# Performance work log

Hardware: AMD Instinct MI355X
Metric: run time of the kernel (lower is better)

## Reference

```python
import math
import jax, jax.numpy as jnp
import numpy as np

GRAIN = 300   # bilinear / grain dim (gpconv output channels)
PAD = 4       # explicit zero padding before each conv1d / conv2d
POOL = 40     # adaptive pool target (mf_model_pool_dim)

def conv1d_k2(x, w, b):
    # x: [B, L, Cin], w: [Cout, Cin, 2] -> [B, L-1, Cout]
    return (jnp.einsum('blc,oc->blo', x[:, :-1], w[:, :, 0])
            + jnp.einsum('blc,oc->blo', x[:, 1:], w[:, :, 1]) + b)

def kmax_last(x, k):
    # torch-style k-max pooling: top-k values along last axis, original order kept
    idx = jnp.sort(jax.lax.top_k(x, k)[1], axis=-1)
    return jnp.take_along_axis(x, idx, axis=-1)

def kmax_len(x, k):
    # k-max pooling over the length axis (axis=1) of [B, L, C]
    return jnp.swapaxes(kmax_last(jnp.swapaxes(x, 1, 2), k), 1, 2)

def adaptive_max_1d(x, out, axis):
    # torch AdaptiveMaxPool semantics along one axis; windows precomputed statically
    L = x.shape[axis]
    r = np.arange(out)
    starts = (r * L) // out
    ends = -((-(r + 1) * L) // out)
    maxw = int((ends - starts).max())
    off = starts[:, None] + np.arange(maxw)[None, :]
    mask = jnp.asarray(off < ends[:, None])
    idxs = np.minimum(off, L - 1)
    xm = jnp.moveaxis(x, axis, -1)
    g = jnp.where(mask, xm[..., idxs], -jnp.inf)
    return jnp.moveaxis(g.max(-1), -1, axis)

def conv2d_p4(x, w, b):
    y = jax.lax.conv_general_dilated(x, w, (1, 1), [(PAD, PAD), (PAD, PAD)],
                                     dimension_numbers=('NCHW', 'OIHW', 'NCHW'))
    return y + b[None, :, None, None]

def gp_tower(x, w1, b1, w2, b2, w3, b3, k1, k2):
    # multigranular conv tower: zero-pad(4) -> conv1d(k=2) -> tanh -> k-max pool
    g0 = kmax_last(x, GRAIN)                      # [B, L, 300]
    def block(z, w, b, k):
        z = jnp.pad(z, ((0, 0), (PAD, PAD), (0, 0)))
        return kmax_len(jnp.tanh(conv1d_k2(z, w, b)), k)
    p1 = block(x, w1, b1, k1)                     # [B, k1, 300]
    p2 = block(p1, w2, b2, k2)                    # [B, k2, 300]
    p3 = block(p2, w3, b3, 1)                     # [B, 1, 300]
    return jnp.concatenate([g0, p1, p2, p3], axis=1)

def _forward(query, pos_doc, neg_docs, qw1, qb1, qw2, qb2, qw3, qb3,
             dw1, db1, dw2, db2, dw3, db3, bw, bb,
             mw1, mb1, mw2, mb2, mw3, mb3, lw, lb):
    B, Lq, _ = query.shape
    S, _, Ld, _ = neg_docs.shape
    kq1, kq2 = max(4, math.ceil(2 * Lq / 3)), max(4, math.ceil(Lq / 3))
    kd1, kd2 = max(4, math.ceil(2 * Ld / 3)), max(4, math.ceil(Ld / 3))
    qg = gp_tower(query, qw1, qb1, qw2, qb2, qw3, qb3, kq1, kq2)   # [B, Nq, 300]
    docs = jnp.concatenate([pos_doc[None], neg_docs], 0).reshape((S + 1) * B, Ld, -1)
    dg = gp_tower(docs, dw1, db1, dw2, db2, dw3, db3, kd1, kd2)    # [(S+1)B, Nd, 300]
    Nq, Nd = qg.shape[1], dg.shape[1]
    dg = dg.reshape(S + 1, B, Nd, GRAIN)
    # batched bilinear matching + sigmoid (replaces the O(Nq*Nd) per-pair loop)
    qt = jnp.einsum('bqd,de->bqe', qg, bw)
    M = jax.nn.sigmoid(jnp.einsum('bqe,sbje->sbqj', qt, dg) + bb[0])
    M = M.reshape((S + 1) * B, Nq, Nd)
    x = adaptive_max_1d(adaptive_max_1d(M, POOL, 1), POOL, 2)[:, None]  # [N,1,40,40]
    for w, b in ((mw1, mb1), (mw2, mb2), (mw3, mb3)):
        x = jax.nn.sigmoid(conv2d_p4(x, w, b))
        x = adaptive_max_1d(adaptive_max_1d(x, POOL, 2), POOL, 3)
        x = x.max(axis=1, keepdims=True)          # k-max(k=1) over channels
    feat = x[:, 0]                                # [N, 40, 40]
    h = jax.nn.sigmoid(jnp.einsum('nij,j->ni', feat, lw[0]) + lb[0])
    s = jax.nn.sigmoid(h @ lw[0] + lb[0])
    return s.reshape(S + 1, B)                    # row 0 = pos-doc scores

def setup_inputs():
    ks = jax.random.split(jax.random.key(0), 26)
    def n(i, shape, s=0.05):
        return jax.random.normal(ks[i], shape, dtype=jnp.float32) * s
    return dict(
        query=jax.random.normal(ks[0], (16, 239, 1024), dtype=jnp.float32),
        pos_doc=jax.random.normal(ks[1], (16, 479, 1024), dtype=jnp.float32),
        neg_docs=jax.random.normal(ks[2], (4, 16, 479, 1024), dtype=jnp.float32),
        qw1=n(3, (300, 1024, 2)), qb1=n(4, (300,)),
        qw2=n(5, (300, 300, 2)), qb2=n(6, (300,)),
        qw3=n(7, (300, 300, 2)), qb3=n(8, (300,)),
        dw1=n(9, (300, 1024, 2)), db1=n(10, (300,)),
        dw2=n(11, (300, 300, 2)), db2=n(12, (300,)),
        dw3=n(13, (300, 300, 2)), db3=n(14, (300,)),
        bw=n(15, (300, 300)), bb=n(16, (1,)),
        mw1=n(17, (50, 1, 2, 2)), mb1=n(18, (50,)),
        mw2=n(19, (50, 1, 2, 2)), mb2=n(20, (50,)),
        mw3=n(21, (50, 1, 2, 2)), mb3=n(22, (50,)),
        lw=n(23, (1, 40)), lb=n(24, (1,)),
    )

def reference(query, pos_doc, neg_docs, qw1, qb1, qw2, qb2, qw3, qb3,
              dw1, db1, dw2, db2, dw3, db3, bw, bb,
              mw1, mb1, mw2, mb2, mw3, mb3, lw, lb):
    return _forward(query, pos_doc, neg_docs, qw1, qb1, qw2, qb2, qw3, qb3,
                    dw1, db1, dw2, db2, dw3, db3, bw, bb,
                    mw1, mb1, mw2, mb2, mw3, mb3, lw, lb)
```

## Files before the change

kernel.cpp:

```cpp
#include <hip/hip_runtime.h>
#include <hip/hip_bf16.h>
#include <math.h>

typedef unsigned long long ull;
typedef unsigned int uint;
typedef unsigned short ushort_t;

typedef short bf16x8 __attribute__((ext_vector_type(8)));
typedef float floatx4 __attribute__((ext_vector_type(4)));

__device__ inline ushort_t f2b(float f) {
    uint u = __float_as_uint(f);
    u = u + 0x7fffu + ((u >> 16) & 1u);
    return (ushort_t)(u >> 16);
}

__device__ inline uint kmap16(ushort_t u) {
    return (u & 0x8000u) ? (uint)((~u) & 0xFFFFu) : (uint)(u | 0x8000u);
}
__device__ inline ushort_t kinv16(uint k) {
    return (k & 0x8000u) ? (ushort_t)(k ^ 0x8000u) : (ushort_t)((~k) & 0xFFFFu);
}

__device__ inline void async_copy16(const void* g, void* l) {
    __builtin_amdgcn_global_load_lds(
        (const __attribute__((address_space(1))) void*)g,
        (__attribute__((address_space(3))) void*)l, 16, 0, 0);
}

__global__ void prep_w2_kernel(const float* __restrict__ w, ushort_t* __restrict__ Wb,
                               int C, int CP) {
    int CHn = CP / 32;
    int total = CHn * 2 * 20 * 512;
    for (int i = blockIdx.x * blockDim.x + threadIdx.x; i < total;
         i += gridDim.x * blockDim.x) {
        int e = i & 7;
        int lane = (i >> 3) & 63;
        int rest = i >> 9;
        int g = rest % 20;
        int tc = rest / 20;
        int t = tc & 1, c = tc >> 1;
        int o = g * 16 + (lane & 15);
        int ch = c * 32 + (lane >> 4) * 8 + e;
        float v = (o < 300 && ch < C) ? w[((size_t)o * C + ch) * 2 + t] : 0.f;
        Wb[i] = f2b(v);
    }
}

__global__ void prep_bw_kernel(const float* __restrict__ bw, ushort_t* __restrict__ bwb) {
    int i = blockIdx.x * 256 + threadIdx.x;
    if (i >= 320 * 320) return;
    int e = i / 320, d = i - e * 320;
    bwb[i] = (e < 300 && d < 300) ? f2b(bw[d * 300 + e]) : (ushort_t)0;
}

__global__ __launch_bounds__(256) void x_pad_bf16_kernel(
    const float* __restrict__ src, const float* __restrict__ src2, int split_n,
    long long s_nstr, int Lin, ushort_t* __restrict__ dst, int rows)
{
    int r = blockIdx.x, n = blockIdx.y;
    const float* sp = (split_n > 0 && n >= split_n)
                          ? src2 + (size_t)(n - split_n) * s_nstr
                          : src + (size_t)n * s_nstr;
    int g = r - 4;
    ushort_t* dp = dst + ((size_t)n * rows + r) * 1024;
    int c = threadIdx.x * 4;
    ushort4 o = {0, 0, 0, 0};
    if (g >= 0 && g < Lin) {
        float4 v = *(const float4*)&sp[(size_t)g * 1024 + c];
        o.x = f2b(v.x); o.y = f2b(v.y); o.z = f2b(v.z); o.w = f2b(v.w);
    }
    *(ushort4*)&dp[c] = o;
}

template <int CP>
__global__ __launch_bounds__(256, 2) void conv_lds_kernel(
    const ushort_t* __restrict__ xq, long long xq_nstr,
    const ushort_t* __restrict__ xd, long long xd_nstr,
    const ushort_t* __restrict__ Wq, const ushort_t* __restrict__ Wd,
    const float* __restrict__ bq, const float* __restrict__ bd,
    int Lout_q, int Lout_d, int mtiles_q,
    ushort_t* __restrict__ yt)
{
    constexpr int CH = CP / 32;
    constexpr int BUFB = 65 * 64;
    __shared__ ushort_t Abuf[3][65 * 32];

    int mt = blockIdx.x, n = blockIdx.y;
    bool isq = (n < 16);
    if (isq && mt >= mtiles_q) return;
    const ushort_t* x = isq ? xq + (size_t)n * xq_nstr
                            : xd + (size_t)(n - 16) * xd_nstr;
    const ushort_t* W = isq ? Wq : Wd;
    const float* bias = isq ? bq : bd;
    int Lout = isq ? Lout_q : Lout_d;
    int l0 = mt * 64;

    int tid = threadIdx.x, wid = tid >> 6, lane = tid & 63;
    int wn = wid * 80;
    int lrow = lane & 15, quad = lane >> 4;

    int srow = tid >> 2;
    int sslot = (tid & 3) ^ ((tid >> 3) & 3);
    const ushort_t* gMain = x + (size_t)(l0 + srow) * CP + sslot * 8;
    const ushort_t* gXtra = x + (size_t)(l0 + 64) * CP + wid * 8;

    const ushort_t* Bw = W + ((size_t)wid * 5) * 512 + lane * 8;

    int offA[2][4];
#pragma unroll
    for (int t = 0; t < 2; t++)
#pragma unroll
        for (int ms = 0; ms < 4; ms++) {
            int r = ms * 16 + lrow + t;
            offA[t][ms] = r * 64 + ((quad ^ ((r >> 1) & 3)) << 4);
        }

    floatx4 acc[4][5];
#pragma unroll
    for (int i = 0; i < 4; i++)
#pragma unroll
        for (int j = 0; j < 5; j++) acc[i][j] = (floatx4){0.f, 0.f, 0.f, 0.f};

    char* lds0 = (char*)&Abuf[0][0];

    auto STAGE = [&](int cc, int slot) {
        char* lb = lds0 + slot * BUFB;
        async_copy16(gMain + cc * 32, lb + wid * 1024);
        if (lane == 0) async_copy16(gXtra + cc * 32, lb + 4096 + wid * 16);
    };
    auto LOADB = [&](bf16x8 (&bf)[2][5], int cc) {
#pragma unroll
        for (int t = 0; t < 2; t++)
#pragma unroll
            for (int ns = 0; ns < 5; ns++)
                bf[t][ns] = *(const bf16x8*)(Bw + (size_t)((cc * 2 + t) * 20 + ns) * 512);
    };
    auto COMPUTE = [&](bf16x8 (&bf)[2][5], int rslot) {
        const char* ab = lds0 + rslot * BUFB;
        __builtin_amdgcn_s_setprio(1);
#pragma unroll
        for (int t = 0; t < 2; t++) {
            bf16x8 af[4];
#pragma unroll
            for (int ms = 0; ms < 4; ms++)
                af[ms] = *(const bf16x8*)(ab + offA[t][ms]);
#pragma unroll
            for (int ms = 0; ms < 4; ms++)
#pragma unroll
                for (int ns = 0; ns < 5; ns++)
                    acc[ms][ns] = __builtin_amdgcn_mfma_f32_16x16x32_bf16(
                        af[ms], bf[t][ns], acc[ms][ns], 0, 0, 0);
        }
        __builtin_amdgcn_s_setprio(0);
    };
    auto WAITBAR = [&]() {
        asm volatile("s_waitcnt vmcnt(10)" ::: "memory");
        __builtin_amdgcn_s_barrier();
        __builtin_amdgcn_sched_barrier(0);
    };

    bf16x8 bA[2][5], bB[2][5];

    STAGE(0, 0);
    LOADB(bA, 0);
    STAGE(1, 1);

    int sl = 0;
    for (int c = 0; c < CH; c += 2) {
        int rA = sl;
        int rB = rA + 1; if (rB == 3) rB = 0;
        int wA = rB + 1; if (wA == 3) wA = 0;
        int wB = rA;

        WAITBAR();
        LOADB(bB, c + 1);
        __builtin_amdgcn_sched_barrier(0x38F);
        if (c + 2 < CH) STAGE(c + 2, wA);
        COMPUTE(bA, rA);

        WAITBAR();
        if (c + 2 < CH) LOADB(bA, c + 2);
        __builtin_amdgcn_sched_barrier(0x38F);
        if (c + 3 < CH) STAGE(c + 3, wB);
        COMPUTE(bB, rB);

        sl = wA;
    }

    ushort_t* yp = yt + (size_t)n * (320 * 488);
#pragma unroll
    for (int ns = 0; ns < 5; ns++) {
        int o = wn + ns * 16 + lrow;
        if (o >= 300) continue;
        float bo = bias[o];
        ushort_t* orow = yp + (size_t)o * 488;
#pragma unroll
        for (int ms = 0; ms < 4; ms++) {
            int l = l0 + ms * 16 + quad * 4;
            if (l + 3 < Lout) {
                ushort4 v;
                v.x = f2b(tanhf(acc[ms][ns][0] + bo));
                v.y = f2b(tanhf(acc[ms][ns][1] + bo));
                v.z = f2b(tanhf(acc[ms][ns][2] + bo));
                v.w = f2b(tanhf(acc[ms][ns][3] + bo));
                *(ushort4*)&orow[l] = v;
            } else {
#pragma unroll
                for (int r = 0; r < 4; r++)
                    if (l + r < Lout) orow[l + r] = f2b(tanhf(acc[ms][ns][r] + bo));
            }
        }
    }
}

__global__ __launch_bounds__(256) void topk_g0_kernel(
    const ushort_t* __restrict__ src, int CC, long long s_n,
    ushort_t* __restrict__ out, long long o_n, long long o_c)
{
    __shared__ uint hist[4][257];

    int tid = threadIdx.x, wid = tid >> 6, lane = tid & 63;
    int row = blockIdx.x * 4 + wid;
    int n = row / CC, c = row - n * CC;
    const ushort_t* sp = src + (size_t)n * s_n + (size_t)c * 1024;

    const uint* sp32 = (const uint*)(sp + (size_t)lane * 16);
    uint pk[8];
    {
        uint4 va = *(const uint4*)sp32;
        uint4 vb = *(const uint4*)(sp32 + 4);
        pk[0] = va.x; pk[1] = va.y; pk[2] = va.z; pk[3] = va.w;
        pk[4] = vb.x; pk[5] = vb.y; pk[6] = vb.z; pk[7] = vb.w;
    }
    uint key[16];
#pragma unroll
    for (int i = 0; i < 8; i++) {
        uint w = pk[i];
        uint s = w & 0x80008000u;
        w ^= 0x80008000u | ((s >> 15) * 0x7fffu);
        key[2 * i] = w & 0xffffu;
        key[2 * i + 1] = w >> 16;
    }

    uint* hg = hist[wid];
    uint rem = 300, bsel = 0, T = 0;

#pragma unroll
    for (int round = 0; round < 2; round++) {
#pragma unroll
        for (int t = 0; t < 4; t++) hg[lane + t * 64] = 0;
        __builtin_amdgcn_sched_barrier(0);
        if (round == 0) {
#pragma unroll
            for (int e = 0; e < 16; e++) atomicAdd(&hg[key[e] >> 8], 1u);
        } else {
#pragma unroll
            for (int e = 0; e < 16; e++)
                if ((key[e] >> 8) == bsel) atomicAdd(&hg[key[e] & 255u], 1u);
        }
        __builtin_amdgcn_sched_barrier(0);
        uint hv[4], Sr = 0;
#pragma unroll
        for (int t = 0; t < 4; t++) { hv[t] = hg[lane * 4 + t]; Sr += hv[t]; }
        uint suf = Sr;
#pragma unroll
        for (int off = 1; off < 64; off <<= 1) {
            uint u = __shfl_down(suf, off);
            if (lane + off < 64) suf += u;
        }
        uint acc = suf - Sr;
        uint found = 0;
#pragma unroll
        for (int t = 3; t >= 0; t--) {
            uint h = hv[t];
            if (!found && acc < rem && acc + h >= rem)
                found = ((uint)(lane * 4 + t) << 16) | (rem - acc);
            acc += h;
        }
#pragma unroll
        for (int off = 1; off < 64; off <<= 1) found |= __shfl_xor(found, off);
        if (round == 0) {
            bsel = found >> 16;
            rem = found & 0xffffu;
        } else {
            T = (bsel << 8) | (found >> 16);
            rem = found & 0xffffu;
        }
        __builtin_amdgcn_sched_barrier(0);
    }

    uint gtc = 0, eqc = 0;
#pragma unroll
    for (int e = 0; e < 16; e++) {
        gtc += (key[e] > T) ? 1u : 0u;
        eqc += (key[e] == T) ? 1u : 0u;
    }
    uint pack = (gtc << 16) | eqc, incl = pack;
#pragma unroll
    for (int off = 1; off < 64; off <<= 1) {
        uint u = __shfl_up(incl, off);
        if (lane >= off) incl += u;
    }
    uint excl = incl - pack;
    uint gt_b = excl >> 16, eq_b = excl & 0xffffu;

    ushort_t* dp = out + (size_t)n * o_n + (size_t)c * o_c;
#pragma unroll
    for (int e = 0; e < 16; e++) {
        uint kk = key[e];
        if (kk > T) {
            uint pos = gt_b + (eq_b < rem ? eq_b : rem);
            dp[pos] = kinv16(kk);
            gt_b++;
        } else if (kk == T) {
            if (eq_b < rem) dp[gt_b + eq_b] = kinv16(kk);
            eq_b++;
        }
    }
}

__global__ __launch_bounds__(256) void topk_cols_kernel(
    const ushort_t* __restrict__ yt2,
    int Lq, int Ld, int kq, int kd,
    ushort_t* __restrict__ qg, int qoff,
    ushort_t* __restrict__ dg, int doff,
    ushort_t* __restrict__ pq, long long pq_nstr,
    ushort_t* __restrict__ pd, long long pd_nstr)
{
    __shared__ __align__(16) ushort_t xin[32][488];
    __shared__ __align__(16) uint hist[32 * 257];
    ushort_t* otile = (ushort_t*)hist;

    int cg = blockIdx.x, n = blockIdx.y;
    int c0 = cg * 32;
    bool isq = (n < 16);
    int L = isq ? Lq : Ld;
    int k = isq ? kq : kd;
    int nd = isq ? n : n - 16;
    int tid = threadIdx.x;

    const ushort_t* src = yt2 + (size_t)n * (320 * 488) + (size_t)c0 * 488;
    for (int i = tid; i < 32 * 61; i += 256) {
        int j = i / 61, s = i - j * 61;
        *(uint4*)&xin[j][s * 8] = *(const uint4*)&src[(size_t)j * 488 + s * 8];
    }
    __syncthreads();

    int g = tid >> 3, r = tid & 7;
    uint* hg = &hist[g * 257];
    bool cval = (c0 + g) < 300;
    int S = (L + 7) >> 3;
    int llo = r * S, lhi = llo + S;
    if (lhi > L) lhi = L;
    if (llo > L) llo = L;

    uint rem = (uint)k;
    uint bsel = 0;
    uint Tt = 0;

#pragma unroll
    for (int round = 0; round < 2; round++) {
        for (int t = r; t < 256; t += 8) hg[t] = 0;
        for (int l = llo; l < lhi; l++) {
            uint key = cval ? kmap16(xin[g][l]) : 0x8000u;
            if (round == 0)
                atomicAdd(&hg[key >> 8], 1u);
            else if ((key >> 8) == bsel)
                atomicAdd(&hg[key & 255u], 1u);
        }
        uint hv[32];
        uint Sr = 0;
        int b0 = r * 32;
#pragma unroll
        for (int t = 0; t < 32; t++) { hv[t] = hg[b0 + t]; Sr += hv[t]; }
        uint suf = Sr;
#pragma unroll
        for (int off = 1; off < 8; off <<= 1) {
            uint u = __shfl_down(suf, off);
            if (r + off < 8) suf += u;
        }
        uint acc = suf - Sr;
        uint found = 0;
#pragma unroll
        for (int t = 31; t >= 0; t--) {
            uint h = hv[t];
            if (!found && acc < rem && acc + h >= rem)
                found = ((uint)(b0 + t) << 16) | (rem - acc);
            acc += h;
        }
#pragma unroll
        for (int off = 1; off < 8; off <<= 1) found |= __shfl_xor(found, off);
        if (round == 0) {
            bsel = found >> 16;
            rem = found & 0xffffu;
        } else {
            Tt = (bsel << 8) | (found >> 16);
            rem = found & 0xffffu;
        }
    }

    uint gtc = 0, eqc = 0;
    for (int l = llo; l < lhi; l++) {
        uint key = cval ? kmap16(xin[g][l]) : 0x8000u;
        gtc += (key > Tt) ? 1u : 0u;
        eqc += (key == Tt) ? 1u : 0u;
    }
    uint pack = (gtc << 16) | eqc, incl = pack;
#pragma unroll
    for (int off = 1; off < 8; off <<= 1) {
        uint u = __shfl_up(incl, off);
        if (r >= off) incl += u;
    }
    uint excl = incl - pack;
    uint gt_b = excl >> 16, eq_b = excl & 0xffffu;

    __syncthreads();

    for (int l = llo; l < lhi; l++) {
        uint key = cval ? kmap16(xin[g][l]) : 0x8000u;
        if (key > Tt) {
            uint pos = gt_b + (eq_b < rem ? eq_b : rem);
            otile[pos * 32 + g] = kinv16(key);
            gt_b++;
        } else if (key == Tt) {
            if (eq_b < rem) otile[(gt_b + eq_b) * 32 + g] = kinv16(key);
            eq_b++;
        }
    }
    __syncthreads();

    ushort_t* d1 = isq ? qg + ((size_t)nd * 480 + qoff) * 320 + c0
                       : dg + ((size_t)nd * 960 + doff) * 320 + c0;
    ushort_t* d2 = 0;
    if (isq) { if (pq) d2 = pq + (size_t)nd * pq_nstr + 4 * 320 + c0; }
    else     { if (pd) d2 = pd + (size_t)nd * pd_nstr + 4 * 320 + c0; }

    for (int i = tid; i < k * 8; i += 256) {
        int p = i >> 3, s = i & 7;
        ushort4 v = *(ushort4*)&otile[p * 32 + s * 4];
        *(ushort4*)&d1[(size_t)p * 320 + s * 4] = v;
        if (d2) *(ushort4*)&d2[(size_t)p * 320 + s * 4] = v;
    }
}

__global__ __launch_bounds__(256) void qt_mfma_kernel(
    const ushort_t* __restrict__ qgb, const ushort_t* __restrict__ bwb,
    ushort_t* __restrict__ qtb)
{
    int mt = blockIdx.x, b = blockIdx.y;
    int tid = threadIdx.x, wid = tid >> 6, lane = tid & 63;
    int wn = wid * 80, lrow = lane & 15, quad = lane >> 4;

    const ushort_t* A = qgb + ((size_t)b * 480 + mt * 48 + lrow) * 320 + quad * 8;
    const ushort_t* B = bwb + (size_t)(wn + lrow) * 320 + quad * 8;

    floatx4 acc[3][5];
#pragma unroll
    for (int i = 0; i < 3; i++)
#pragma unroll
        for (int j = 0; j < 5; j++) acc[i][j] = (floatx4){0.f, 0.f, 0.f, 0.f};

#pragma unroll 5
    for (int c0 = 0; c0 < 320; c0 += 32) {
        bf16x8 af[3], bfr[5];
#pragma unroll
        for (int ms = 0; ms < 3; ms++)
            af[ms] = *(const bf16x8*)&A[(size_t)(ms * 16) * 320 + c0];
#pragma unroll
        for (int ns = 0; ns < 5; ns++)
            bfr[ns] = *(const bf16x8*)&B[(size_t)(ns * 16) * 320 + c0];
#pragma unroll
        for (int ms = 0; ms < 3; ms++)
#pragma unroll
            for (int ns = 0; ns < 5; ns++)
                acc[ms][ns] = __builtin_amdgcn_mfma_f32_16x16x32_bf16(
                    af[ms], bfr[ns], acc[ms][ns], 0, 0, 0);
    }

    ushort_t* out = qtb + ((size_t)b * 480 + mt * 48) * 320;
#pragma unroll
    for (int ms = 0; ms < 3; ms++)
#pragma unroll
        for (int ns = 0; ns < 5; ns++)
#pragma unroll
            for (int r = 0; r < 4; r++)
                out[(size_t)(ms * 16 + quad * 4 + r) * 320 + wn + ns * 16 + lrow] =
                    f2b(acc[ms][ns][r]);
}

__global__ __launch_bounds__(256) void mpool_mfma_kernel(
    const ushort_t* __restrict__ qtb16, const ushort_t* __restrict__ dgb16,
    const float* __restrict__ bb, float* __restrict__ mp)
{
    __shared__ float pool[2 * 12 * 192];

    int jb = blockIdx.x;
    int qb = blockIdx.y;
    int n  = blockIdx.z;
    int b  = n & 15;

    int tid = threadIdx.x;
    int wid = tid >> 6, lane = tid & 63;
    int wm2 = wid >> 1;
    int wm = wm2 * 48, wn = (wid & 1) * 96;
    int lrow = lane & 15, quad = lane >> 4;

    const ushort_t* Abase = qtb16 + ((size_t)b * 480 + qb * 96 + wm) * 320 + quad * 8;
    const ushort_t* Bbase = dgb16 + ((size_t)n * 960 + jb * 192 + wn) * 320 + quad * 8;

    floatx4 acc[3][6];
#pragma unroll
    for (int i = 0; i < 3; i++)
#pragma unroll
        for (int j = 0; j < 6; j++) acc[i][j] = (floatx4){0.f, 0.f, 0.f, 0.f};

#pragma unroll 2
    for (int c0 = 0; c0 < 320; c0 += 32) {
        bf16x8 af[3], bfr[6];
#pragma unroll
        for (int mt = 0; mt < 3; mt++)
            af[mt] = *(const bf16x8*)&Abase[(size_t)(mt * 16 + lrow) * 320 + c0];
#pragma unroll
        for (int nt = 0; nt < 6; nt++)
            bfr[nt] = *(const bf16x8*)&Bbase[(size_t)(nt * 16 + lrow) * 320 + c0];
#pragma unroll
        for (int mt = 0; mt < 3; mt++)
#pragma unroll
            for (int nt = 0; nt < 6; nt++)
                acc[mt][nt] = __builtin_amdgcn_mfma_f32_16x16x32_bf16(
                    af[mt], bfr[nt], acc[mt][nt], 0, 0, 0);
    }

#pragma unroll
    for (int mt = 0; mt < 3; mt++) {
        int g = mt * 4 + quad;
#pragma unroll
        for (int nt = 0; nt < 6; nt++) {
            floatx4 a = acc[mt][nt];
            float rm = fmaxf(fmaxf(a[0], a[1]), fmaxf(a[2], a[3]));
            pool[(wm2 * 12 + g) * 192 + wn + nt * 16 + lrow] = rm;
        }
    }
    __syncthreads();

    if (tid < 64) {
        int qw = tid >> 3, jw = tid & 7;
        int slab = qw >> 2, w = qw & 3;
        float m = -INFINITY;
        const float* pp = &pool[(slab * 12 + w * 3) * 192 + jw * 24];
        for (int g = 0; g < 3; g++)
            for (int cc = 0; cc < 24; cc++)
                m = fmaxf(m, pp[g * 192 + cc]);
        float sig = 1.f / (1.f + expf(-(m + bb[0])));
        mp[(size_t)n * 1600 + (size_t)(qb * 8 + qw) * 40 + (jb * 8 + jw)] = sig;
    }
}

#define OCG 10
__global__ __launch_bounds__(256) void convblock_atomic_kernel(
    const float* __restrict__ X, const float* __restrict__ w,
    const float* __restrict__ bias, uint* __restrict__ Y)
{
    __shared__ float xp[48 * 48];
    __shared__ float ys[47 * 47];
    __shared__ float t1[40 * 47];
    __shared__ float outacc[1600];

    int n = blockIdx.x, t = threadIdx.x;
    int oc0 = blockIdx.y * OCG;
    const float* xn = X + (size_t)n * 1600;
    for (int i = t; i < 48 * 48; i += 256) {
        int r = i / 48, c = i - r * 48;
        int rr = r - 4, cc = c - 4;
        xp[i] = (rr >= 0 && rr < 40 && cc >= 0 && cc < 40) ? xn[rr * 40 + cc] : 0.f;
    }
    for (int i = t; i < 1600; i += 256) outacc[i] = 0.f;
    __syncthreads();

    for (int oc = oc0; oc < oc0 + OCG; oc++) {
        float w00 = w[oc * 4 + 0], w01 = w[oc * 4 + 1];
        float w10 = w[oc * 4 + 2], w11 = w[oc * 4 + 3];
        float bo = bias[oc];
        for (int i = t; i < 47 * 47; i += 256) {
            int r = i / 47, c = i - r * 47;
            float v = xp[r * 48 + c] * w00 + xp[r * 48 + c + 1] * w01
                    + xp[(r + 1) * 48 + c] * w10 + xp[(r + 1) * 48 + c + 1] * w11 + bo;
            ys[i] = 1.f / (1.f + expf(-v));
        }
        __syncthreads();
        for (int i = t; i < 40 * 47; i += 256) {
            int r = i / 47, c = i - r * 47;
            int s = (47 * r) / 40, e = (47 * (r + 1) + 39) / 40;
            float m = ys[s * 47 + c];
            for (int x = s + 1; x < e; x++) m = fmaxf(m, ys[x * 47 + c]);
            t1[i] = m;
        }
        __syncthreads();
        for (int i = t; i < 1600; i += 256) {
            int r = i / 40, c = i - r * 40;
            int s = (47 * c) / 40, e = (47 * (c + 1) + 39) / 40;
            float m = t1[r * 47 + s];
            for (int x = s + 1; x < e; x++) m = fmaxf(m, t1[r * 47 + x]);
            outacc[i] = fmaxf(outacc[i], m);
        }
        __syncthreads();
    }
    for (int i = t; i < 1600; i += 256)
        atomicMax(&Y[(size_t)n * 1600 + i], __float_as_uint(outacc[i]));
}

__global__ __launch_bounds__(64) void head_kernel(
    const float* __restrict__ feat, const float* __restrict__ lw,
    const float* __restrict__ lb, float* __restrict__ out)
{
    __shared__ float hs[40];
    int n = blockIdx.x, t = threadIdx.x;
    const float* f = feat + (size_t)n * 1600;
    if (t < 40) {
        float a = 0.f;
        for (int j = 0; j < 40; j++) a += f[t * 40 + j] * lw[j];
        hs[t] = 1.f / (1.f + expf(-(a + lb[0])));
    }
    __syncthreads();
    if (t == 0) {
        float a = 0.f;
        for (int i = 0; i < 40; i++) a += hs[i] * lw[i];
        out[n] = 1.f / (1.f + expf(-(a + lb[0])));
    }
}

extern "C" void kernel_launch(void* const* d_in, const int* in_sizes, int n_in,
                              void* d_out, int out_size, void* d_ws, size_t ws_size,
                              hipStream_t stream) {
    const float* query    = (const float*)d_in[0];
    const float* pos_doc  = (const float*)d_in[1];
    const float* neg_docs = (const float*)d_in[2];
    const float* qw1 = (const float*)d_in[3];  const float* qb1 = (const float*)d_in[4];
    const float* qw2 = (const float*)d_in[5];  const float* qb2 = (const float*)d_in[6];
    const float* qw3 = (const float*)d_in[7];  const float* qb3 = (const float*)d_in[8];
    const float* dw1 = (const float*)d_in[9];  const float* db1 = (const float*)d_in[10];
    const float* dw2 = (const float*)d_in[11]; const float* db2 = (const float*)d_in[12];
    const float* dw3 = (const float*)d_in[13]; const float* db3 = (const float*)d_in[14];
    const float* bw  = (const float*)d_in[15]; const float* bb  = (const float*)d_in[16];
    const float* mw1 = (const float*)d_in[17]; const float* mb1 = (const float*)d_in[18];
    const float* mw2 = (const float*)d_in[19]; const float* mb2 = (const float*)d_in[20];
    const float* mw3 = (const float*)d_in[21]; const float* mb3 = (const float*)d_in[22];
    const float* lw  = (const float*)d_in[23]; const float* lb  = (const float*)d_in[24];

    float* ws = (float*)d_ws;
    ushort_t* qw1b  = (ushort_t*)(ws + 0);
    ushort_t* qw2b  = (ushort_t*)(ws + 327680);
    ushort_t* qw3b  = (ushort_t*)(ws + 430080);
    ushort_t* dw1b  = (ushort_t*)(ws + 532480);
    ushort_t* dw2b  = (ushort_t*)(ws + 860160);
    ushort_t* dw3b  = (ushort_t*)(ws + 962560);
    ushort_t* bwb   = (ushort_t*)(ws + 1064960);
    ushort_t* qgb16 = (ushort_t*)(ws + 1116160);
    ushort_t* dgb16 = (ushort_t*)(ws + 2344960);
    ushort_t* yt    = (ushort_t*)(ws + 14632960);
    ushort_t* qxb   = (ushort_t*)(ws + 22128640);
    ushort_t* p1q   = (ushort_t*)(ws + 22128640);
    ushort_t* p2q   = (ushort_t*)(ws + 22640640);
    ushort_t* dxb   = (ushort_t*)(ws + 24291328);
    ushort_t* p1d   = (ushort_t*)(ws + 24291328);
    ushort_t* p2d   = (ushort_t*)(ws + 28899328);
    ushort_t* qtb16 = (ushort_t*)(ws + 31459328);
    float*    mp    = ws + 32688128;
    float*    ya    = ws + 32816128;
    float*    yb    = ws + 32944128;
    float*    yc    = ws + 33072128;

    prep_w2_kernel<<<1280, 256, 0, stream>>>(qw1, qw1b, 1024, 1024);
    prep_w2_kernel<<<400, 256, 0, stream>>>(qw2, qw2b, 300, 320);
    prep_w2_kernel<<<400, 256, 0, stream>>>(qw3, qw3b, 300, 320);
    prep_w2_kernel<<<1280, 256, 0, stream>>>(dw1, dw1b, 1024, 1024);
    prep_w2_kernel<<<400, 256, 0, stream>>>(dw2, dw2b, 300, 320);
    prep_w2_kernel<<<400, 256, 0, stream>>>(dw3, dw3b, 300, 320);
    prep_bw_kernel<<<400, 256, 0, stream>>>(bw, bwb);

    {
        dim3 g(264, 16);
        x_pad_bf16_kernel<<<g, 256, 0, stream>>>(query, nullptr, 0,
                                                 239LL * 1024, 239, qxb, 264);
    }
    {
        dim3 g(520, 80);
        x_pad_bf16_kernel<<<g, 256, 0, stream>>>(pos_doc, neg_docs, 16,
                                                 479LL * 1024, 479, dxb, 520);
    }

    topk_g0_kernel<<<(16 * 239) / 4, 256, 0, stream>>>(
        qxb + 4 * 1024, 239, 264LL * 1024, qgb16, 480LL * 320, 320);
    topk_g0_kernel<<<(80 * 479) / 4, 256, 0, stream>>>(
        dxb + 4 * 1024, 479, 520LL * 1024, dgb16, 960LL * 320, 320);

    {
        dim3 g(8, 96);
        conv_lds_kernel<1024><<<g, 256, 0, stream>>>(
            qxb, 264LL * 1024, dxb, 520LL * 1024,
            qw1b, dw1b, qb1, db1, 246, 486, 4, yt);
    }

    hipMemsetAsync(p1q, 0, 16 * 200 * 320 * 2, stream);
    hipMemsetAsync(p2q, 0, 16 * 104 * 320 * 2, stream);
    hipMemsetAsync(p1d, 0, (size_t)80 * 360 * 320 * 2, stream);
    hipMemsetAsync(p2d, 0, (size_t)80 * 200 * 320 * 2, stream);
    hipMemsetAsync(ya, 0, 80 * 1600 * 4, stream);
    hipMemsetAsync(yb, 0, 80 * 1600 * 4, stream);
    hipMemsetAsync(yc, 0, 80 * 1600 * 4, stream);

    {
        dim3 g(10, 96);
        topk_cols_kernel<<<g, 256, 0, stream>>>(
            yt, 246, 486, 160, 320,
            qgb16, 239, dgb16, 479,
            p1q, 200LL * 320, p1d, 360LL * 320);
    }

    {
        dim3 g(6, 96);
        conv_lds_kernel<320><<<g, 256, 0, stream>>>(
            p1q, 200LL * 320, p1d, 360LL * 320,
            qw2b, dw2b, qb2, db2, 167, 327, 3, yt);
    }

    {
        dim3 g(10, 96);
        topk_cols_kernel<<<g, 256, 0, stream>>>(
            yt, 167, 327, 80, 160,
            qgb16, 399, dgb16, 799,
            p2q, 104LL * 320, p2d, 200LL * 320);
    }

    {
        dim3 g(3, 96);
        conv_lds_kernel<320><<<g, 256, 0, stream>>>(
            p2q, 104LL * 320, p2d, 200LL * 320,
            qw3b, dw3b, qb3, db3, 87, 167, 2, yt);
    }

    {
        dim3 g(10, 96);
        topk_cols_kernel<<<g, 256, 0, stream>>>(
            yt, 87, 167, 1, 1,
            qgb16, 479, dgb16, 959,
            nullptr, 0, nullptr, 0);
    }

    {
        dim3 g(10, 16);
        qt_mfma_kernel<<<g, 256, 0, stream>>>(qgb16, bwb, qtb16);
    }
    {
        dim3 g(5, 5, 80);
        mpool_mfma_kernel<<<g, 256, 0, stream>>>(qtb16, dgb16, bb, mp);
    }

    {
        dim3 g(80, 5);
        convblock_atomic_kernel<<<g, 256, 0, stream>>>(mp, mw1, mb1, (uint*)ya);
        convblock_atomic_kernel<<<g, 256, 0, stream>>>(ya, mw2, mb2, (uint*)yb);
        convblock_atomic_kernel<<<g, 256, 0, stream>>>(yb, mw3, mb3, (uint*)yc);
    }
    head_kernel<<<80, 64, 0, stream>>>(yc, lw, lb, (float*)d_out);
}
```

Measured before the change: 1.101 ms.

## Restructure conv kernels so each wave owns an independent 64x64 output tile

```diff
diff --git a/kernel.cpp b/kernel.cpp
--- a/kernel.cpp
+++ b/kernel.cpp
@@ -74,38 +74,43 @@
 }
 
 template <int CP>
-__global__ __launch_bounds__(256, 2) void conv_lds_kernel(
+__global__ __launch_bounds__(256, 3) void conv_wave_kernel(
     const ushort_t* __restrict__ xq, long long xq_nstr,
     const ushort_t* __restrict__ xd, long long xd_nstr,
     const ushort_t* __restrict__ Wq, const ushort_t* __restrict__ Wd,
     const float* __restrict__ bq, const float* __restrict__ bd,
-    int Lout_q, int Lout_d, int mtiles_q,
+    int Lout_q, int Lout_d, int mtiles_q, int mtiles_d,
     ushort_t* __restrict__ yt)
 {
     constexpr int CH = CP / 32;
-    constexpr int BUFB = 65 * 64;
-    __shared__ ushort_t Abuf[3][65 * 32];
-
-    int mt = blockIdx.x, n = blockIdx.y;
-    bool isq = (n < 16);
-    if (isq && mt >= mtiles_q) return;
-    const ushort_t* x = isq ? xq + (size_t)n * xq_nstr
-                            : xd + (size_t)(n - 16) * xd_nstr;
-    const ushort_t* W = isq ? Wq : Wd;
-    const float* bias = isq ? bq : bd;
-    int Lout = isq ? Lout_q : Lout_d;
+    __shared__ char Abuf[4][3][4160];
+
+    int tid = threadIdx.x, wid = tid >> 6, lane = tid & 63;
+    int u = blockIdx.x * 4 + wid;
+    int md5 = mtiles_d * 5, DOCU = md5 * 80;
+
+    const ushort_t* x; const ushort_t* W; const float* bias;
+    int Lout, mt, nt, ng;
+    if (u < DOCU) {
+        int nd = u / md5, r = u - nd * md5;
+        mt = r / 5; nt = r - mt * 5;
+        x = xd + (size_t)nd * xd_nstr; W = Wd; bias = bd; Lout = Lout_d;
+        ng = 16 + nd;
+    } else {
+        int v = u - DOCU, mq5 = mtiles_q * 5;
+        int nq = v / mq5, r = v - nq * mq5;
+        mt = r / 5; nt = r - mt * 5;
+        x = xq + (size_t)nq * xq_nstr; W = Wq; bias = bq; Lout = Lout_q;
+        ng = nq;
+    }
     int l0 = mt * 64;
-
-    int tid = threadIdx.x, wid = tid >> 6, lane = tid & 63;
-    int wn = wid * 80;
     int lrow = lane & 15, quad = lane >> 4;
 
-    int srow = tid >> 2;
-    int sslot = (tid & 3) ^ ((tid >> 3) & 3);
-    const ushort_t* gMain = x + (size_t)(l0 + srow) * CP + sslot * 8;
-    const ushort_t* gXtra = x + (size_t)(l0 + 64) * CP + wid * 8;
-
-    const ushort_t* Bw = W + ((size_t)wid * 5) * 512 + lane * 8;
+    const ushort_t* gMain = x + (size_t)(l0 + (lane >> 2)) * CP
+                              + ((lane & 3) ^ ((lane >> 3) & 3)) * 8;
+    const ushort_t* gXtra = x + (size_t)(l0 + 64) * CP + lane * 8;
+
+    const ushort_t* Bw = W + (size_t)(nt * 4) * 512 + lane * 8;
 
     int offA[2][4];
 #pragma unroll
@@ -116,28 +121,43 @@
             offA[t][ms] = r * 64 + ((quad ^ ((r >> 1) & 3)) << 4);
         }
 
-    floatx4 acc[4][5];
+    floatx4 acc[4][4];
 #pragma unroll
     for (int i = 0; i < 4; i++)
 #pragma unroll
-        for (int j = 0; j < 5; j++) acc[i][j] = (floatx4){0.f, 0.f, 0.f, 0.f};
-
-    char* lds0 = (char*)&Abuf[0][0];
+        for (int j = 0; j < 4; j++) acc[i][j] = (floatx4){0.f, 0.f, 0.f, 0.f};
+
+    char* lb0 = &Abuf[wid][0][0];
 
     auto STAGE = [&](int cc, int slot) {
-        char* lb = lds0 + slot * BUFB;
-        async_copy16(gMain + cc * 32, lb + wid * 1024);
-        if (lane == 0) async_copy16(gXtra + cc * 32, lb + 4096 + wid * 16);
+        char* lb = lb0 + slot * 4160;
+        const ushort_t* gs = gMain + cc * 32;
+        async_copy16(gs, lb);
+        async_copy16(gs + (size_t)16 * CP, lb + 1024);
+        async_copy16(gs + (size_t)32 * CP, lb + 2048);
+        async_copy16(gs + (size_t)48 * CP, lb + 3072);
+        if (lane < 4) async_copy16(gXtra + cc * 32, lb + 4096);
     };
-    auto LOADB = [&](bf16x8 (&bf)[2][5], int cc) {
+
+    STAGE(0, 0);
+    STAGE(1, 1);
+
+    for (int c = 0; c < CH; c++) {
+        if (c == 0) asm volatile("s_waitcnt vmcnt(5)" ::: "memory");
+        else        asm volatile("s_waitcnt vmcnt(8)" ::: "memory");
+        __builtin_amdgcn_sched_barrier(0);
+
+        bf16x8 bf[2][4];
 #pragma unroll
         for (int t = 0; t < 2; t++)
 #pragma unroll
-            for (int ns = 0; ns < 5; ns++)
-                bf[t][ns] = *(const bf16x8*)(Bw + (size_t)((cc * 2 + t) * 20 + ns) * 512);
-    };
-    auto COMPUTE = [&](bf16x8 (&bf)[2][5], int rslot) {
-        const char* ab = lds0 + rslot * BUFB;
+            for (int ns = 0; ns < 4; ns++)
+                bf[t][ns] = *(const bf16x8*)(Bw + (size_t)((c * 2 + t) * 20 + ns) * 512);
+        __builtin_amdgcn_sched_barrier(0x38F);
+
+        if (c + 2 < CH) STAGE(c + 2, (c + 2) % 3);
+
+        const char* ab = lb0 + (c % 3) * 4160;
         __builtin_amdgcn_s_setprio(1);
 #pragma unroll
         for (int t = 0; t < 2; t++) {
@@ -148,50 +168,17 @@
 #pragma unroll
             for (int ms = 0; ms < 4; ms++)
 #pragma unroll
-                for (int ns = 0; ns < 5; ns++)
+                for (int ns = 0; ns < 4; ns++)
                     acc[ms][ns] = __builtin_amdgcn_mfma_f32_16x16x32_bf16(
                         af[ms], bf[t][ns], acc[ms][ns], 0, 0, 0);
         }
         __builtin_amdgcn_s_setprio(0);
-    };
-    auto WAITBAR = [&]() {
-        asm volatile("s_waitcnt vmcnt(10)" ::: "memory");
-        __builtin_amdgcn_s_barrier();
-        __builtin_amdgcn_sched_barrier(0);
-    };
-
-    bf16x8 bA[2][5], bB[2][5];
-
-    STAGE(0, 0);
-    LOADB(bA, 0);
-    STAGE(1, 1);
-
-    int sl = 0;
-    for (int c = 0; c < CH; c += 2) {
-        int rA = sl;
-        int rB = rA + 1; if (rB == 3) rB = 0;
-        int wA = rB + 1; if (wA == 3) wA = 0;
-        int wB = rA;
-
-        WAITBAR();
-        LOADB(bB, c + 1);
-        __builtin_amdgcn_sched_barrier(0x38F);
-        if (c + 2 < CH) STAGE(c + 2, wA);
-        COMPUTE(bA, rA);
-
-        WAITBAR();
-        if (c + 2 < CH) LOADB(bA, c + 2);
-        __builtin_amdgcn_sched_barrier(0x38F);
-        if (c + 3 < CH) STAGE(c + 3, wB);
-        COMPUTE(bB, rB);
-
-        sl = wA;
-    }
-
-    ushort_t* yp = yt + (size_t)n * (320 * 488);
-#pragma unroll
-    for (int ns = 0; ns < 5; ns++) {
-        int o = wn + ns * 16 + lrow;
+    }
+
+    ushort_t* yp = yt + (size_t)ng * (320 * 488);
+#pragma unroll
+    for (int ns = 0; ns < 4; ns++) {
+        int o = nt * 64 + ns * 16 + lrow;
         if (o >= 300) continue;
         float bo = bias[o];
         ushort_t* orow = yp + (size_t)o * 488;
@@ -695,12 +682,9 @@
     topk_g0_kernel<<<(80 * 479) / 4, 256, 0, stream>>>(
         dxb + 4 * 1024, 479, 520LL * 1024, dgb16, 960LL * 320, 320);
 
-    {
-        dim3 g(8, 96);
-        conv_lds_kernel<1024><<<g, 256, 0, stream>>>(
-            qxb, 264LL * 1024, dxb, 520LL * 1024,
-            qw1b, dw1b, qb1, db1, 246, 486, 4, yt);
-    }
+    conv_wave_kernel<1024><<<880, 256, 0, stream>>>(
+        qxb, 264LL * 1024, dxb, 520LL * 1024,
+        qw1b, dw1b, qb1, db1, 246, 486, 4, 8, yt);
 
     hipMemsetAsync(p1q, 0, 16 * 200 * 320 * 2, stream);
     hipMemsetAsync(p2q, 0, 16 * 104 * 320 * 2, stream);
@@ -718,12 +702,9 @@
             p1q, 200LL * 320, p1d, 360LL * 320);
     }
 
-    {
-        dim3 g(6, 96);
-        conv_lds_kernel<320><<<g, 256, 0, stream>>>(
-            p1q, 200LL * 320, p1d, 360LL * 320,
-            qw2b, dw2b, qb2, db2, 167, 327, 3, yt);
-    }
+    conv_wave_kernel<320><<<660, 256, 0, stream>>>(
+        p1q, 200LL * 320, p1d, 360LL * 320,
+        qw2b, dw2b, qb2, db2, 167, 327, 3, 6, yt);
 
     {
         dim3 g(10, 96);
@@ -733,12 +714,9 @@
             p2q, 104LL * 320, p2d, 200LL * 320);
     }
 
-    {
-        dim3 g(3, 96);
-        conv_lds_kernel<320><<<g, 256, 0, stream>>>(
-            p2q, 104LL * 320, p2d, 200LL * 320,
-            qw3b, dw3b, qb3, db3, 87, 167, 2, yt);
-    }
+    conv_wave_kernel<320><<<340, 256, 0, stream>>>(
+        p2q, 104LL * 320, p2d, 200LL * 320,
+        qw3b, dw3b, qb3, db3, 87, 167, 2, 3, yt);
 
     {
         dim3 g(10, 96);
```

New measurement: 1.074 ms. -2.4%, faster.
